# Performance work log

Measured on AMD Instinct MI355X. Metric: run time of the kernel, lower is better.

## Reference

```python
import jax, jax.numpy as jnp
import numpy as np

N_NODES = 100000
N_EDGES = 1600000
EPS = 1e-5


def _xavier(key, shape):
    fan_out, fan_in = shape
    lim = float(np.sqrt(6.0 / (fan_in + fan_out)))
    return jax.random.uniform(key, shape, jnp.float32, -lim, lim)


def setup_inputs() -> dict:
    key = jax.random.key(0)
    ks = jax.random.split(key, 16)
    d_in, d1, d2, d3 = 32, 64, 128, 64
    inp = {
        "x": jax.random.normal(ks[0], (N_NODES, d_in), jnp.float32),
        "edge_index": jax.random.randint(ks[1], (2, N_EDGES), 0, N_NODES, jnp.int64),
        "edge_weight": jax.random.uniform(ks[2], (N_EDGES,), jnp.float32),
        # GraphConv params: lin_rel (with bias) applied to aggregated msgs, lin_root (no bias)
        "W1_rel": _xavier(ks[3], (d1, d_in)), "b1": jnp.zeros((d1,), jnp.float32), "W1_root": _xavier(ks[4], (d1, d_in)),
        "W2_rel": _xavier(ks[5], (d2, d1)), "b2": jnp.zeros((d2,), jnp.float32), "W2_root": _xavier(ks[6], (d2, d1)),
        "W3_rel": _xavier(ks[7], (d3, d2)), "b3": jnp.zeros((d3,), jnp.float32), "W3_root": _xavier(ks[8], (d3, d2)),
        # BatchNorm affine params
        "g1": jnp.ones((d1,), jnp.float32), "be1": jnp.zeros((d1,), jnp.float32),
        "g2": jnp.ones((d2,), jnp.float32), "be2": jnp.zeros((d2,), jnp.float32),
        "g3": jnp.ones((d3,), jnp.float32), "be3": jnp.zeros((d3,), jnp.float32),
        # node-level classifier: Linear(64,32) -> ReLU -> Linear(32,2)
        "Wc1": _xavier(ks[9], (32, d3)), "bc1": jnp.zeros((32,), jnp.float32),
        "Wc2": _xavier(ks[10], (2, 32)), "bc2": jnp.zeros((2,), jnp.float32),
    }
    return inp


def _graph_conv(x, src, dst, W_rel, b, W_root, ew=None):
    msg = x[src]                      # [E, d] gather
    if ew is not None:
        msg = msg * ew[:, None]
    agg = jax.ops.segment_sum(msg, dst, num_segments=N_NODES)  # [N, d] scatter-add
    return agg @ W_rel.T + b + x @ W_root.T


def _bn(h, g, beta):
    mu = jnp.mean(h, axis=0)
    var = jnp.var(h, axis=0)
    return (h - mu) * jax.lax.rsqrt(var + EPS) * g + beta


def reference(x, edge_index, edge_weight,
              W1_rel, b1, W1_root, W2_rel, b2, W2_root, W3_rel, b3, W3_root,
              g1, be1, g2, be2, g3, be3, Wc1, bc1, Wc2, bc2):
    src, dst = edge_index[0], edge_index[1]
    h1 = jax.nn.relu(_bn(_graph_conv(x, src, dst, W1_rel, b1, W1_root), g1, be1))
    h2 = jax.nn.relu(_bn(_graph_conv(h1, src, dst, W2_rel, b2, W2_root), g2, be2))
    h3 = _bn(_graph_conv(h2, src, dst, W3_rel, b3, W3_root, edge_weight), g3, be3)
    h3 = jax.nn.relu(h3 + h1)  # residual (dims match, no projection)
    logits = jax.nn.relu(h3 @ Wc1.T + bc1) @ Wc2.T + bc2  # [N, 2]
    return logits
```

## Files before the change

### kernel.cpp

```cpp
#include <hip/hip_runtime.h>

#define N_NODES 100000
#define N_EDGES 1600000
#define EPSV 1e-5f

__device__ __forceinline__ ushort f2bf(float f) {
  unsigned u = __float_as_uint(f);
  unsigned r = (u + 0x7FFFu + ((u >> 16) & 1u)) >> 16;
  return (ushort)r;
}


#define FILL_SUB 256
#define GRP_W 12500

__global__ void hist_kernel(const int* __restrict__ ei, int* __restrict__ cnt) {
  const int g = blockIdx.x & 7;
  const int sub = blockIdx.x >> 3;
  const int lo = g * GRP_W, hi = lo + GRP_W;
  const int EPB = (N_EDGES + FILL_SUB - 1) / FILL_SUB;
  const int beg = sub * EPB;
  const int end = min(beg + EPB, N_EDGES);
  for (int e = beg + (int)threadIdx.x; e < end; e += (int)blockDim.x) {
    int d = __builtin_nontemporal_load(ei + N_EDGES + e);
    if (d >= lo && d < hi) atomicAdd(&cnt[d], 1);
  }
}

#define SCAN_BLK 1024
#define SCAN_NB ((N_NODES + SCAN_BLK - 1) / SCAN_BLK)

__global__ void scan_phase1(const int* __restrict__ cnt, int* __restrict__ blocksum) {
  __shared__ int part[256];
  int base = blockIdx.x * SCAN_BLK + threadIdx.x * 4;
  int s = 0;
#pragma unroll
  for (int i = 0; i < 4; ++i) {
    int idx = base + i;
    if (idx < N_NODES) s += cnt[idx];
  }
  part[threadIdx.x] = s;
  __syncthreads();
  for (int d = 128; d > 0; d >>= 1) {
    if (threadIdx.x < d) part[threadIdx.x] += part[threadIdx.x + d];
    __syncthreads();
  }
  if (threadIdx.x == 0) blocksum[blockIdx.x] = part[0];
}

__global__ void scan_phase2(int* __restrict__ blocksum, int* __restrict__ rowptr) {
  __shared__ int part[128];
  int tid = threadIdx.x;
  int v = (tid < SCAN_NB) ? blocksum[tid] : 0;
  part[tid] = v;
  __syncthreads();
  for (int d = 1; d < 128; d <<= 1) {
    int t = (tid >= d) ? part[tid - d] : 0;
    __syncthreads();
    part[tid] += t;
    __syncthreads();
  }
  if (tid < SCAN_NB) blocksum[tid] = part[tid] - v;
  if (tid == 127) rowptr[N_NODES] = part[127];
}

__global__ void scan_phase3(const int* __restrict__ cnt, const int* __restrict__ blocksum,
                            int* __restrict__ rowptr, int* __restrict__ cursor) {
  __shared__ int part[256];
  int base = blockIdx.x * SCAN_BLK + threadIdx.x * 4;
  int c[4];
  int s = 0;
#pragma unroll
  for (int i = 0; i < 4; ++i) {
    int idx = base + i;
    c[i] = (idx < N_NODES) ? cnt[idx] : 0;
    s += c[i];
  }
  part[threadIdx.x] = s;
  __syncthreads();
  int me = s;
  for (int d = 1; d < 256; d <<= 1) {
    int t = (threadIdx.x >= d) ? part[threadIdx.x - d] : 0;
    __syncthreads();
    part[threadIdx.x] += t;
    __syncthreads();
  }
  int off = blocksum[blockIdx.x] + part[threadIdx.x] - me;
#pragma unroll
  for (int i = 0; i < 4; ++i) {
    int idx = base + i;
    if (idx < N_NODES) {
      rowptr[idx] = off;
      cursor[idx] = off;
      off += c[i];
    }
  }
}

__global__ void fill_kernel(const int* __restrict__ ei, const float* __restrict__ ew,
                            int* __restrict__ cursor, unsigned* __restrict__ col) {
  const int g = blockIdx.x & 7;
  const int sub = blockIdx.x >> 3;
  const int lo = g * GRP_W, hi = lo + GRP_W;
  const int EPB = (N_EDGES + FILL_SUB - 1) / FILL_SUB;
  const int beg = sub * EPB;
  const int end = min(beg + EPB, N_EDGES);
  for (int e = beg + (int)threadIdx.x; e < end; e += (int)blockDim.x) {
    int d = __builtin_nontemporal_load(ei + N_EDGES + e);
    if (d < lo || d >= hi) continue;
    int p = atomicAdd(&cursor[d], 1);
    int src = __builtin_nontemporal_load(ei + e);
    float w = __builtin_nontemporal_load(ew + e);
    col[p] = ((unsigned)f2bf(w) << 17) | (unsigned)src;
  }
}


__global__ void cast_bf16(const float* __restrict__ in, ushort* __restrict__ out, int n4) {
  int i = blockIdx.x * blockDim.x + threadIdx.x;
  if (i >= n4) return;
  float4 v = reinterpret_cast<const float4*>(in)[i];
  ushort4 o = make_ushort4(f2bf(v.x), f2bf(v.y), f2bf(v.z), f2bf(v.w));
  reinterpret_cast<ushort4*>(out)[i] = o;
}


__global__ void wtrans_kernel(const float* __restrict__ W1rel, const float* __restrict__ W1root,
                              const float* __restrict__ W2rel, const float* __restrict__ W2root,
                              const float* __restrict__ W3rel, const float* __restrict__ W3root,
                              float* __restrict__ Wt) {
  int i = blockIdx.x * blockDim.x + threadIdx.x;
  if (i >= 36864) return;
  float v;
  if (i < 4096) {
    int k = i >> 6, j = i & 63;
    v = (k < 32) ? W1rel[j * 32 + k] : W1root[j * 32 + (k - 32)];
  } else if (i < 20480) {
    int r = i - 4096;
    int k = r >> 7, j = r & 127;
    v = (k < 64) ? W2rel[j * 64 + k] : W2root[j * 64 + (k - 64)];
  } else if (i < 28672) {
    int r = i - 20480;
    int k = r >> 6, j = r & 63;
    v = W3rel[j * 128 + k];
  } else {
    int r = i - 28672;
    int k = r >> 6, j = r & 63;
    v = W3root[j * 128 + k];
  }
  Wt[i] = v;
}


#define SRC_OF(v) ((v) & 0x1FFFFu)
#define W_OF(v) __uint_as_float(((v) >> 17) << 16)

__device__ __forceinline__ unsigned pack2bf(float a, float b) {
  return (unsigned)f2bf(a) | ((unsigned)f2bf(b) << 16);
}

__global__ void gather_d32_bf(const ushort* __restrict__ xb, const int* __restrict__ rowptr,
                              const unsigned* __restrict__ col, ushort* __restrict__ agg) {
  int gid = blockIdx.x * blockDim.x + threadIdx.x;
  int n = gid >> 2;
  if (n >= N_NODES) return;
  int c = gid & 3;
  int beg = rowptr[n], end = rowptr[n + 1];
  float acc[8];
#pragma unroll
  for (int i = 0; i < 8; ++i) acc[i] = 0.f;

  auto body = [&](const uint4& u) {
    unsigned uu[4] = {u.x, u.y, u.z, u.w};
#pragma unroll
    for (int i = 0; i < 4; ++i) {
      acc[2 * i]     += __uint_as_float(uu[i] << 16);
      acc[2 * i + 1] += __uint_as_float(uu[i] & 0xFFFF0000u);
    }
  };

  int p = beg;
  for (; p + 3 < end; p += 4) {
    unsigned e0 = col[p], e1 = col[p + 1], e2 = col[p + 2], e3 = col[p + 3];
    uint4 u0 = *reinterpret_cast<const uint4*>(xb + (size_t)SRC_OF(e0) * 32 + c * 8);
    uint4 u1 = *reinterpret_cast<const uint4*>(xb + (size_t)SRC_OF(e1) * 32 + c * 8);
    uint4 u2 = *reinterpret_cast<const uint4*>(xb + (size_t)SRC_OF(e2) * 32 + c * 8);
    uint4 u3 = *reinterpret_cast<const uint4*>(xb + (size_t)SRC_OF(e3) * 32 + c * 8);
    body(u0); body(u1); body(u2); body(u3);
  }
  for (; p < end; ++p) {
    unsigned e0 = col[p];
    uint4 u0 = *reinterpret_cast<const uint4*>(xb + (size_t)SRC_OF(e0) * 32 + c * 8);
    body(u0);
  }
  uint4 o = make_uint4(pack2bf(acc[0], acc[1]), pack2bf(acc[2], acc[3]),
                       pack2bf(acc[4], acc[5]), pack2bf(acc[6], acc[7]));
  *reinterpret_cast<uint4*>(agg + (size_t)n * 32 + c * 8) = o;
}

template <bool WEIGHTED, bool TRANS, bool OUTB16>
__global__ void gather_d64_bf(const ushort* __restrict__ hb, const int* __restrict__ rowptr,
                              const unsigned* __restrict__ col,
                              const float* __restrict__ sc, const float* __restrict__ sh,
                              void* __restrict__ aggv) {
  int gid = blockIdx.x * blockDim.x + threadIdx.x;
  int n = gid >> 3;
  if (n >= N_NODES) return;
  int c = gid & 7;
  int beg = rowptr[n], end = rowptr[n + 1];
  float sc8[8], sh8[8];
  if (TRANS) {
#pragma unroll
    for (int i = 0; i < 8; ++i) {
      sc8[i] = sc[c * 8 + i];
      sh8[i] = sh[c * 8 + i];
    }
  }
  float acc[8];
#pragma unroll
  for (int i = 0; i < 8; ++i) acc[i] = 0.f;

  auto body = [&](unsigned ev, const uint4& u) {
    float w = WEIGHTED ? W_OF(ev) : 1.f;
    unsigned uu[4] = {u.x, u.y, u.z, u.w};
#pragma unroll
    for (int i = 0; i < 4; ++i) {
      float lo = __uint_as_float(uu[i] << 16);
      float hi = __uint_as_float(uu[i] & 0xFFFF0000u);
      if (TRANS) {
        lo = fmaxf(fmaf(lo, sc8[2 * i], sh8[2 * i]), 0.f);
        hi = fmaxf(fmaf(hi, sc8[2 * i + 1], sh8[2 * i + 1]), 0.f);
      }
      if (WEIGHTED) {
        acc[2 * i]     = fmaf(lo, w, acc[2 * i]);
        acc[2 * i + 1] = fmaf(hi, w, acc[2 * i + 1]);
      } else {
        acc[2 * i]     += lo;
        acc[2 * i + 1] += hi;
      }
    }
  };

  int p = beg;
  for (; p + 3 < end; p += 4) {
    unsigned e0 = col[p], e1 = col[p + 1], e2 = col[p + 2], e3 = col[p + 3];
    uint4 u0 = *reinterpret_cast<const uint4*>(hb + (size_t)SRC_OF(e0) * 64 + c * 8);
    uint4 u1 = *reinterpret_cast<const uint4*>(hb + (size_t)SRC_OF(e1) * 64 + c * 8);
    uint4 u2 = *reinterpret_cast<const uint4*>(hb + (size_t)SRC_OF(e2) * 64 + c * 8);
    uint4 u3 = *reinterpret_cast<const uint4*>(hb + (size_t)SRC_OF(e3) * 64 + c * 8);
    body(e0, u0); body(e1, u1); body(e2, u2); body(e3, u3);
  }
  for (; p < end; ++p) {
    unsigned e0 = col[p];
    uint4 u0 = *reinterpret_cast<const uint4*>(hb + (size_t)SRC_OF(e0) * 64 + c * 8);
    body(e0, u0);
  }
  if constexpr (OUTB16) {
    uint4 o = make_uint4(pack2bf(acc[0], acc[1]), pack2bf(acc[2], acc[3]),
                         pack2bf(acc[4], acc[5]), pack2bf(acc[6], acc[7]));
    *reinterpret_cast<uint4*>((ushort*)aggv + (size_t)n * 64 + c * 8) = o;
  } else {
    float* op = (float*)aggv + (size_t)n * 64 + c * 8;
    *reinterpret_cast<float4*>(op)     = make_float4(acc[0], acc[1], acc[2], acc[3]);
    *reinterpret_cast<float4*>(op + 4) = make_float4(acc[4], acc[5], acc[6], acc[7]);
  }
}


template <int K1, int K2, int DO, int A1B16, int A2B16, int TA1, int TA2, int RADD,
          int STATS, int OUTM>
__global__ __launch_bounds__(256, 4) void gemm_node(
    const void* __restrict__ A1v, const void* __restrict__ A2v,
    const float* __restrict__ Wt,
    const float* __restrict__ sc, const float* __restrict__ sh,
    const float* __restrict__ R, float* __restrict__ out, ushort* __restrict__ outb,
    float* __restrict__ sums) {
  constexpr int K = K1 + K2;
  constexpr int NC = K / 32;
  constexpr int NJB = DO / 64;
  __shared__ __align__(16) float A_lds[64][36];
  __shared__ __align__(16) float W_lds[32][DO];

  const int tid = threadIdx.x;
  const int tx = tid & 15, ty = tid >> 4;
  const int nbase = blockIdx.x * 64;

  float4 acc[4][NJB];
#pragma unroll
  for (int i = 0; i < 4; ++i)
#pragma unroll
    for (int jb = 0; jb < NJB; ++jb) acc[i][jb] = make_float4(0.f, 0.f, 0.f, 0.f);

#pragma unroll 1
  for (int c = 0; c < NC; ++c) {
    const int kb = c * 32;
    if (c) __syncthreads();
#pragma unroll
    for (int it = 0; it < 2; ++it) {
      int idx = it * 256 + tid;
      int nl = idx >> 3;
      int kq = (idx & 7) * 4;
      int k = kb + kq;
      int ng = nbase + nl;
      float4 v = make_float4(0.f, 0.f, 0.f, 0.f);
      bool isA1 = (K2 == 0) || (k < K1);
      if (ng < N_NODES) {
        if (isA1) {
          if constexpr (A1B16) {
            uint2 u = *reinterpret_cast<const uint2*>(
                (const ushort*)A1v + (size_t)ng * K1 + k);
            v.x = __uint_as_float(u.x << 16);
            v.y = __uint_as_float(u.x & 0xFFFF0000u);
            v.z = __uint_as_float(u.y << 16);
            v.w = __uint_as_float(u.y & 0xFFFF0000u);
          } else {
            v = *reinterpret_cast<const float4*>((const float*)A1v + (size_t)ng * K1 + k);
          }
        } else {
          if constexpr (A2B16) {
            uint2 u = *reinterpret_cast<const uint2*>(
                (const ushort*)A2v + (size_t)ng * K2 + (k - K1));
            v.x = __uint_as_float(u.x << 16);
            v.y = __uint_as_float(u.x & 0xFFFF0000u);
            v.z = __uint_as_float(u.y << 16);
            v.w = __uint_as_float(u.y & 0xFFFF0000u);
          } else {
            v = *reinterpret_cast<const float4*>(
                (const float*)A2v + (size_t)ng * K2 + (k - K1));
          }
        }
      }
      if constexpr (TA1) {
        if (isA1) {
          float4 s4 = *reinterpret_cast<const float4*>(sc + k);
          float4 h4 = *reinterpret_cast<const float4*>(sh + k);
          v.x = fmaxf(fmaf(v.x, s4.x, h4.x), 0.f);
          v.y = fmaxf(fmaf(v.y, s4.y, h4.y), 0.f);
          v.z = fmaxf(fmaf(v.z, s4.z, h4.z), 0.f);
          v.w = fmaxf(fmaf(v.w, s4.w, h4.w), 0.f);
        }
      }
      if constexpr (TA2 && K2 > 0) {
        if (!isA1) {
          float4 s4 = *reinterpret_cast<const float4*>(sc + (k - K1));
          float4 h4 = *reinterpret_cast<const float4*>(sh + (k - K1));
          v.x = fmaxf(fmaf(v.x, s4.x, h4.x), 0.f);
          v.y = fmaxf(fmaf(v.y, s4.y, h4.y), 0.f);
          v.z = fmaxf(fmaf(v.z, s4.z, h4.z), 0.f);
          v.w = fmaxf(fmaf(v.w, s4.w, h4.w), 0.f);
        }
      }
      *reinterpret_cast<float4*>(&A_lds[nl][kq]) = v;
    }
    {
      const float4* wsrc = reinterpret_cast<const float4*>(Wt + (size_t)kb * DO);
      float4* wdst = reinterpret_cast<float4*>(&W_lds[0][0]);
#pragma unroll
      for (int it = 0; it < DO / 32; ++it)
        wdst[it * 256 + tid] = wsrc[it * 256 + tid];
    }
    __syncthreads();
#pragma unroll 2
    for (int k4 = 0; k4 < 8; ++k4) {
      float4 a[4];
#pragma unroll
      for (int i = 0; i < 4; ++i)
        a[i] = *reinterpret_cast<const float4*>(&A_lds[ty * 4 + i][k4 * 4]);
#pragma unroll
      for (int q = 0; q < 4; ++q) {
#pragma unroll
        for (int jb = 0; jb < NJB; ++jb) {
          float4 w = *reinterpret_cast<const float4*>(&W_lds[k4 * 4 + q][jb * 64 + tx * 4]);
#pragma unroll
          for (int i = 0; i < 4; ++i) {
            float av = reinterpret_cast<const float*>(&a[i])[q];
            acc[i][jb].x = fmaf(av, w.x, acc[i][jb].x);
            acc[i][jb].y = fmaf(av, w.y, acc[i][jb].y);
            acc[i][jb].z = fmaf(av, w.z, acc[i][jb].z);
            acc[i][jb].w = fmaf(av, w.w, acc[i][jb].w);
          }
        }
      }
    }
  }
#pragma unroll
  for (int i = 0; i < 4; ++i) {
    int ng = nbase + ty * 4 + i;
    if (ng >= N_NODES) continue;
#pragma unroll
    for (int jb = 0; jb < NJB; ++jb) {
      if constexpr (RADD) {
        float4 rr = *reinterpret_cast<const float4*>(R + (size_t)ng * DO + jb * 64 + tx * 4);
        acc[i][jb].x += rr.x; acc[i][jb].y += rr.y;
        acc[i][jb].z += rr.z; acc[i][jb].w += rr.w;
      }
      size_t off = (size_t)ng * DO + jb * 64 + tx * 4;
      if constexpr (OUTM == 1) {
        ushort4 o = make_ushort4(f2bf(acc[i][jb].x), f2bf(acc[i][jb].y),
                                 f2bf(acc[i][jb].z), f2bf(acc[i][jb].w));
        *reinterpret_cast<ushort4*>((ushort*)out + off) = o;
      } else {
        *reinterpret_cast<float4*>(out + off) = acc[i][jb];
        if constexpr (OUTM == 2) {
          ushort4 o = make_ushort4(f2bf(acc[i][jb].x), f2bf(acc[i][jb].y),
                                   f2bf(acc[i][jb].z), f2bf(acc[i][jb].w));
          *reinterpret_cast<ushort4*>(outb + off) = o;
        }
      }
    }
  }
  if constexpr (STATS) {
    __syncthreads();
    float* sums_l = &A_lds[0][0];
    float* sq_l = &W_lds[0][0];
#pragma unroll
    for (int jb = 0; jb < NJB; ++jb) {
      float4 s = make_float4(0.f, 0.f, 0.f, 0.f);
      float4 q = make_float4(0.f, 0.f, 0.f, 0.f);
#pragma unroll
      for (int i = 0; i < 4; ++i) {
        if (nbase + ty * 4 + i < N_NODES) {
          float4 v = acc[i][jb];
          s.x += v.x; s.y += v.y; s.z += v.z; s.w += v.w;
          q.x = fmaf(v.x, v.x, q.x); q.y = fmaf(v.y, v.y, q.y);
          q.z = fmaf(v.z, v.z, q.z); q.w = fmaf(v.w, v.w, q.w);
        }
      }
      *reinterpret_cast<float4*>(&sums_l[ty * DO + jb * 64 + tx * 4]) = s;
      *reinterpret_cast<float4*>(&sq_l[ty * DO + jb * 64 + tx * 4]) = q;
    }
    __syncthreads();
    if (tid < DO) {
      float s = 0.f, q = 0.f;
#pragma unroll
      for (int t = 0; t < 16; ++t) {
        s += sums_l[t * DO + tid];
        q += sq_l[t * DO + tid];
      }
      unsafeAtomicAdd(&sums[tid], s);
      unsafeAtomicAdd(&sums[DO + tid], q);
    }
  }
}


__global__ void bn_finalize(const float* __restrict__ sums, const float* __restrict__ g,
                            const float* __restrict__ be, float* __restrict__ sc,
                            float* __restrict__ sh, int D) {
  int j = threadIdx.x;
  if (j >= D) return;
  const float invN = 1.f / (float)N_NODES;
  float mean = sums[j] * invN;
  float var = sums[D + j] * invN - mean * mean;
  float r = rsqrtf(var + EPSV);
  float scale = g[j] * r;
  sc[j] = scale;
  sh[j] = be[j] - mean * scale;
}


__global__ __launch_bounds__(256) void final_fused(
    const float* __restrict__ h3p, const ushort* __restrict__ h1p,
    const float* __restrict__ sc1, const float* __restrict__ sh1,
    const float* __restrict__ sc3, const float* __restrict__ sh3,
    const float* __restrict__ Wc1, const float* __restrict__ bc1,
    const float* __restrict__ Wc2, const float* __restrict__ bc2,
    float* __restrict__ out) {
  __shared__ __align__(16) float t_lds[64][68];
  __shared__ __align__(16) float w1_lds[64][36];
  __shared__ __align__(16) float c_lds[64][36];
  __shared__ __align__(16) float w2_lds[64];
  __shared__ __align__(16) float b1_lds[32];
  __shared__ float b2_lds[2];
  const int tid = threadIdx.x;
  const int nbase = blockIdx.x * 64;

#pragma unroll
  for (int it = 0; it < 4; ++it) {
    int idx = it * 256 + tid;
    int nl = idx >> 4;
    int k = (idx & 15) * 4;
    int ng = nbase + nl;
    float4 v = make_float4(0.f, 0.f, 0.f, 0.f);
    if (ng < N_NODES) {
      float4 p = *reinterpret_cast<const float4*>(h3p + (size_t)ng * 64 + k);
      uint2 uu = *reinterpret_cast<const uint2*>(h1p + (size_t)ng * 64 + k);
      float ux = __uint_as_float(uu.x << 16);
      float uy = __uint_as_float(uu.x & 0xFFFF0000u);
      float uz = __uint_as_float(uu.y << 16);
      float uw = __uint_as_float(uu.y & 0xFFFF0000u);
      float4 sa = *reinterpret_cast<const float4*>(sc1 + k);
      float4 ha = *reinterpret_cast<const float4*>(sh1 + k);
      float4 sb = *reinterpret_cast<const float4*>(sc3 + k);
      float4 hb = *reinterpret_cast<const float4*>(sh3 + k);
      float h1x = fmaxf(fmaf(ux, sa.x, ha.x), 0.f);
      float h1y = fmaxf(fmaf(uy, sa.y, ha.y), 0.f);
      float h1z = fmaxf(fmaf(uz, sa.z, ha.z), 0.f);
      float h1w = fmaxf(fmaf(uw, sa.w, ha.w), 0.f);
      v.x = fmaxf(fmaf(p.x, sb.x, hb.x) + h1x, 0.f);
      v.y = fmaxf(fmaf(p.y, sb.y, hb.y) + h1y, 0.f);
      v.z = fmaxf(fmaf(p.z, sb.z, hb.z) + h1z, 0.f);
      v.w = fmaxf(fmaf(p.w, sb.w, hb.w) + h1w, 0.f);
    }
    *reinterpret_cast<float4*>(&t_lds[nl][k]) = v;
  }
#pragma unroll
  for (int it = 0; it < 8; ++it) {
    int idx = it * 256 + tid;
    int j = idx >> 6;
    int k = idx & 63;
    w1_lds[k][j] = Wc1[(size_t)j * 64 + k];
  }
  if (tid < 64) w2_lds[tid] = Wc2[tid];
  else if (tid < 96) b1_lds[tid - 64] = bc1[tid - 64];
  else if (tid < 98) b2_lds[tid - 96] = bc2[tid - 96];
  __syncthreads();

  {
    const int tx = tid & 7, ty = tid >> 3;
    float4 a0c = make_float4(0.f, 0.f, 0.f, 0.f);
    float4 a1c = make_float4(0.f, 0.f, 0.f, 0.f);
#pragma unroll 4
    for (int k4 = 0; k4 < 16; ++k4) {
      float4 a0 = *reinterpret_cast<const float4*>(&t_lds[ty * 2 + 0][k4 * 4]);
      float4 a1 = *reinterpret_cast<const float4*>(&t_lds[ty * 2 + 1][k4 * 4]);
#pragma unroll
      for (int q = 0; q < 4; ++q) {
        float4 w = *reinterpret_cast<const float4*>(&w1_lds[k4 * 4 + q][tx * 4]);
        float a0q = reinterpret_cast<const float*>(&a0)[q];
        float a1q = reinterpret_cast<const float*>(&a1)[q];
        a0c.x = fmaf(a0q, w.x, a0c.x); a0c.y = fmaf(a0q, w.y, a0c.y);
        a0c.z = fmaf(a0q, w.z, a0c.z); a0c.w = fmaf(a0q, w.w, a0c.w);
        a1c.x = fmaf(a1q, w.x, a1c.x); a1c.y = fmaf(a1q, w.y, a1c.y);
        a1c.z = fmaf(a1q, w.z, a1c.z); a1c.w = fmaf(a1q, w.w, a1c.w);
      }
    }
    float4 b = *reinterpret_cast<const float4*>(&b1_lds[tx * 4]);
    a0c.x = fmaxf(a0c.x + b.x, 0.f); a0c.y = fmaxf(a0c.y + b.y, 0.f);
    a0c.z = fmaxf(a0c.z + b.z, 0.f); a0c.w = fmaxf(a0c.w + b.w, 0.f);
    a1c.x = fmaxf(a1c.x + b.x, 0.f); a1c.y = fmaxf(a1c.y + b.y, 0.f);
    a1c.z = fmaxf(a1c.z + b.z, 0.f); a1c.w = fmaxf(a1c.w + b.w, 0.f);
    *reinterpret_cast<float4*>(&c_lds[ty * 2 + 0][tx * 4]) = a0c;
    *reinterpret_cast<float4*>(&c_lds[ty * 2 + 1][tx * 4]) = a1c;
  }
  __syncthreads();

  if (tid < 128) {
    int nl = tid >> 1, o = tid & 1;
    int ng = nbase + nl;
    if (ng < N_NODES) {
      float s = b2_lds[o];
#pragma unroll
      for (int k = 0; k < 32; ++k) s = fmaf(c_lds[nl][k], w2_lds[o * 32 + k], s);
      out[(size_t)ng * 2 + o] = s;
    }
  }
}


extern "C" void kernel_launch(void* const* d_in, const int* in_sizes, int n_in,
                              void* d_out, int out_size, void* d_ws, size_t ws_size,
                              hipStream_t stream) {
  const float* x      = (const float*)d_in[0];
  const int*   ei     = (const int*)d_in[1];
  const float* ew     = (const float*)d_in[2];
  const float* W1rel  = (const float*)d_in[3];
  const float* W1root = (const float*)d_in[5];
  const float* W2rel  = (const float*)d_in[6];
  const float* W2root = (const float*)d_in[8];
  const float* W3rel  = (const float*)d_in[9];
  const float* W3root = (const float*)d_in[11];
  const float* g1  = (const float*)d_in[12];
  const float* be1 = (const float*)d_in[13];
  const float* g2  = (const float*)d_in[14];
  const float* be2 = (const float*)d_in[15];
  const float* g3  = (const float*)d_in[16];
  const float* be3 = (const float*)d_in[17];
  const float* Wc1 = (const float*)d_in[18];
  const float* bc1 = (const float*)d_in[19];
  const float* Wc2 = (const float*)d_in[20];
  const float* bc2 = (const float*)d_in[21];

  float* ws = (float*)d_ws;
  const size_t NF = (size_t)N_NODES * 64;
  float* A = ws;
  float* B = ws + NF;
  float* C = ws + 2 * NF;
  float* E = ws + 3 * NF;
  float* X = ws + 5 * NF;
  float* S = X;
  int* rowptr   = (int*)(X + 1024);
  int* cnt      = rowptr + (N_NODES + 2);
  int* cursor   = cnt + N_NODES;
  int* blocksum = cursor + N_NODES;
  unsigned* col = (unsigned*)(blocksum + 128);
  float* Wt     = (float*)(col + N_EDGES);
  float* Wt1  = Wt;
  float* Wt2  = Wt + 4096;
  float* Wt3r = Wt + 20480;
  float* Wt3o = Wt + 28672;

  ushort* agg1b  = (ushort*)A;
  ushort* agg2b  = (ushort*)A;
  ushort* xb     = (ushort*)B;
  ushort* y2b    = (ushort*)B;
  ushort* h1preb = (ushort*)C;
  ushort* h2preb = (ushort*)E;

  hipMemsetAsync(S, 0, 1024 * sizeof(float), stream);
  hipMemsetAsync(cnt, 0, N_NODES * sizeof(int), stream);

  const int tileBlocks = (N_NODES + 63) / 64;

  cast_bf16<<<(N_NODES * 32 / 4 + 255) / 256, 256, 0, stream>>>(x, xb, N_NODES * 32 / 4);
  wtrans_kernel<<<144, 256, 0, stream>>>(W1rel, W1root, W2rel, W2root, W3rel, W3root, Wt);

  hist_kernel<<<8 * FILL_SUB, 256, 0, stream>>>(ei, cnt);
  scan_phase1<<<SCAN_NB, 256, 0, stream>>>(cnt, blocksum);
  scan_phase2<<<1, 128, 0, stream>>>(blocksum, rowptr);
  scan_phase3<<<SCAN_NB, 256, 0, stream>>>(cnt, blocksum, rowptr, cursor);
  fill_kernel<<<8 * FILL_SUB, 256, 0, stream>>>(ei, ew, cursor, col);

  gather_d32_bf<<<(N_NODES * 4 + 255) / 256, 256, 0, stream>>>(xb, rowptr, col, agg1b);
  gemm_node<32, 32, 64, 1, 1, 0, 0, 0, 1, 1><<<tileBlocks, 256, 0, stream>>>(
      agg1b, xb, Wt1, nullptr, nullptr, nullptr, (float*)h1preb, nullptr, S);
  bn_finalize<<<1, 128, 0, stream>>>(S, g1, be1, S + 128, S + 192, 64);

  gather_d64_bf<false, true, true><<<(N_NODES * 8 + 255) / 256, 256, 0, stream>>>(
      h1preb, rowptr, col, S + 128, S + 192, agg2b);
  gemm_node<64, 64, 128, 1, 1, 0, 1, 0, 1, 1><<<tileBlocks, 256, 0, stream>>>(
      agg2b, h1preb, Wt2, S + 128, S + 192, nullptr, (float*)h2preb, nullptr, S + 256);
  bn_finalize<<<1, 128, 0, stream>>>(S + 256, g2, be2, S + 512, S + 640, 128);

  gemm_node<128, 0, 64, 1, 0, 1, 0, 0, 0, 1><<<tileBlocks, 256, 0, stream>>>(
      h2preb, nullptr, Wt3r, S + 512, S + 640, nullptr, (float*)y2b, nullptr, nullptr);

  gather_d64_bf<true, false, false><<<(N_NODES * 8 + 255) / 256, 256, 0, stream>>>(
      y2b, rowptr, col, nullptr, nullptr, A);
  gemm_node<128, 0, 64, 1, 0, 1, 0, 1, 1, 0><<<tileBlocks, 256, 0, stream>>>(
      h2preb, nullptr, Wt3o, S + 512, S + 640, A, B, nullptr, S + 768);
  bn_finalize<<<1, 128, 0, stream>>>(S + 768, g3, be3, S + 896, S + 960, 64);

  final_fused<<<tileBlocks, 256, 0, stream>>>(B, h1preb, S + 128, S + 192, S + 896, S + 960,
                                              Wc1, bc1, Wc2, bc2, (float*)d_out);
}
```

Baseline: 471.6 us.

## Fuse layer-3 rel/root GEMMs and fold root term into weighted gather

Layer 3's rel and root projections now run as one 128-wide GEMM over h2 that writes two bf16 outputs: y2 for the gather and z3 for the root term. The weighted gather adds z3 in its epilogue and stores h3pre as bf16. A new small kernel computes the BN3 statistics from that buffer, and final_fused reads bf16 instead of fp32. This removes one full pass over h2 and the fp32 intermediate traffic, at the cost of an extra stats pass and bf16 rounding of h3pre. The hist and fill kernels also switch to strided uint4 vector loads of the destination indices.

```diff
diff --git a/kernel.cpp b/kernel.cpp
--- a/kernel.cpp
+++ b/kernel.cpp
@@ -18,12 +18,14 @@
   const int g = blockIdx.x & 7;
   const int sub = blockIdx.x >> 3;
   const int lo = g * GRP_W, hi = lo + GRP_W;
-  const int EPB = (N_EDGES + FILL_SUB - 1) / FILL_SUB;
-  const int beg = sub * EPB;
-  const int end = min(beg + EPB, N_EDGES);
-  for (int e = beg + (int)threadIdx.x; e < end; e += (int)blockDim.x) {
-    int d = __builtin_nontemporal_load(ei + N_EDGES + e);
-    if (d >= lo && d < hi) atomicAdd(&cnt[d], 1);
+  const uint4* dst4 = reinterpret_cast<const uint4*>(ei + N_EDGES);
+  const int NV = N_EDGES / 4;
+  for (int i = sub * 256 + (int)threadIdx.x; i < NV; i += FILL_SUB * 256) {
+    uint4 d4 = dst4[i];
+    int dd[4] = {(int)d4.x, (int)d4.y, (int)d4.z, (int)d4.w};
+#pragma unroll
+    for (int j = 0; j < 4; ++j)
+      if (dd[j] >= lo && dd[j] < hi) atomicAdd(&cnt[dd[j]], 1);
   }
 }
 
@@ -102,16 +104,21 @@
   const int g = blockIdx.x & 7;
   const int sub = blockIdx.x >> 3;
   const int lo = g * GRP_W, hi = lo + GRP_W;
-  const int EPB = (N_EDGES + FILL_SUB - 1) / FILL_SUB;
-  const int beg = sub * EPB;
-  const int end = min(beg + EPB, N_EDGES);
-  for (int e = beg + (int)threadIdx.x; e < end; e += (int)blockDim.x) {
-    int d = __builtin_nontemporal_load(ei + N_EDGES + e);
-    if (d < lo || d >= hi) continue;
-    int p = atomicAdd(&cursor[d], 1);
-    int src = __builtin_nontemporal_load(ei + e);
-    float w = __builtin_nontemporal_load(ew + e);
-    col[p] = ((unsigned)f2bf(w) << 17) | (unsigned)src;
+  const uint4* dst4 = reinterpret_cast<const uint4*>(ei + N_EDGES);
+  const int NV = N_EDGES / 4;
+  for (int i = sub * 256 + (int)threadIdx.x; i < NV; i += FILL_SUB * 256) {
+    uint4 d4 = dst4[i];
+    int dd[4] = {(int)d4.x, (int)d4.y, (int)d4.z, (int)d4.w};
+#pragma unroll
+    for (int j = 0; j < 4; ++j) {
+      if (dd[j] >= lo && dd[j] < hi) {
+        int e = i * 4 + j;
+        int p = atomicAdd(&cursor[dd[j]], 1);
+        int src = __builtin_nontemporal_load(ei + e);
+        float w = __builtin_nontemporal_load(ew + e);
+        col[p] = ((unsigned)f2bf(w) << 17) | (unsigned)src;
+      }
+    }
   }
 }
 
@@ -139,14 +146,10 @@
     int r = i - 4096;
     int k = r >> 7, j = r & 127;
     v = (k < 64) ? W2rel[j * 64 + k] : W2root[j * 64 + (k - 64)];
-  } else if (i < 28672) {
+  } else {
     int r = i - 20480;
-    int k = r >> 6, j = r & 63;
-    v = W3rel[j * 128 + k];
-  } else {
-    int r = i - 28672;
-    int k = r >> 6, j = r & 63;
-    v = W3root[j * 128 + k];
+    int k = r >> 7, j = r & 127;
+    v = (j < 64) ? W3rel[(size_t)j * 128 + k] : W3root[(size_t)(j - 64) * 128 + k];
   }
   Wt[i] = v;
 }
@@ -198,11 +201,11 @@
   *reinterpret_cast<uint4*>(agg + (size_t)n * 32 + c * 8) = o;
 }
 
-template <bool WEIGHTED, bool TRANS, bool OUTB16>
+template <bool WEIGHTED, bool TRANS, bool OUTB16, bool ADDZ>
 __global__ void gather_d64_bf(const ushort* __restrict__ hb, const int* __restrict__ rowptr,
                               const unsigned* __restrict__ col,
                               const float* __restrict__ sc, const float* __restrict__ sh,
-                              void* __restrict__ aggv) {
+                              const ushort* __restrict__ zb, void* __restrict__ aggv) {
   int gid = blockIdx.x * blockDim.x + threadIdx.x;
   int n = gid >> 3;
   if (n >= N_NODES) return;
@@ -254,6 +257,15 @@
     unsigned e0 = col[p];
     uint4 u0 = *reinterpret_cast<const uint4*>(hb + (size_t)SRC_OF(e0) * 64 + c * 8);
     body(e0, u0);
+  }
+  if constexpr (ADDZ) {
+    uint4 z = *reinterpret_cast<const uint4*>(zb + (size_t)n * 64 + c * 8);
+    unsigned zz[4] = {z.x, z.y, z.z, z.w};
+#pragma unroll
+    for (int i = 0; i < 4; ++i) {
+      acc[2 * i]     += __uint_as_float(zz[i] << 16);
+      acc[2 * i + 1] += __uint_as_float(zz[i] & 0xFFFF0000u);
+    }
   }
   if constexpr (OUTB16) {
     uint4 o = make_uint4(pack2bf(acc[0], acc[1]), pack2bf(acc[2], acc[3]),
@@ -394,17 +406,24 @@
         acc[i][jb].x += rr.x; acc[i][jb].y += rr.y;
         acc[i][jb].z += rr.z; acc[i][jb].w += rr.w;
       }
-      size_t off = (size_t)ng * DO + jb * 64 + tx * 4;
-      if constexpr (OUTM == 1) {
+      if constexpr (OUTM == 4) {
         ushort4 o = make_ushort4(f2bf(acc[i][jb].x), f2bf(acc[i][jb].y),
                                  f2bf(acc[i][jb].z), f2bf(acc[i][jb].w));
-        *reinterpret_cast<ushort4*>((ushort*)out + off) = o;
+        ushort* dst = (jb == 0) ? (ushort*)out : outb;
+        *reinterpret_cast<ushort4*>(dst + (size_t)ng * 64 + tx * 4) = o;
       } else {
-        *reinterpret_cast<float4*>(out + off) = acc[i][jb];
-        if constexpr (OUTM == 2) {
+        size_t off = (size_t)ng * DO + jb * 64 + tx * 4;
+        if constexpr (OUTM == 1) {
           ushort4 o = make_ushort4(f2bf(acc[i][jb].x), f2bf(acc[i][jb].y),
                                    f2bf(acc[i][jb].z), f2bf(acc[i][jb].w));
-          *reinterpret_cast<ushort4*>(outb + off) = o;
+          *reinterpret_cast<ushort4*>((ushort*)out + off) = o;
+        } else {
+          *reinterpret_cast<float4*>(out + off) = acc[i][jb];
+          if constexpr (OUTM == 2) {
+            ushort4 o = make_ushort4(f2bf(acc[i][jb].x), f2bf(acc[i][jb].y),
+                                     f2bf(acc[i][jb].z), f2bf(acc[i][jb].w));
+            *reinterpret_cast<ushort4*>(outb + off) = o;
+          }
         }
       }
     }
@@ -440,6 +459,31 @@
       unsafeAtomicAdd(&sums[tid], s);
       unsafeAtomicAdd(&sums[DO + tid], q);
     }
+  }
+}
+
+
+__global__ void bn_stats_bf(const ushort* __restrict__ h, float* __restrict__ sums) {
+  __shared__ float sl[256], ql[256];
+  int j = threadIdx.x & 63;
+  int lane = threadIdx.x >> 6;
+  float s = 0.f, q = 0.f;
+  for (int n = blockIdx.x * 4 + lane; n < N_NODES; n += gridDim.x * 4) {
+    float v = __uint_as_float((unsigned)h[(size_t)n * 64 + j] << 16);
+    s += v;
+    q = fmaf(v, v, q);
+  }
+  sl[threadIdx.x] = s;
+  ql[threadIdx.x] = q;
+  __syncthreads();
+  if (threadIdx.x < 64) {
+#pragma unroll
+    for (int t = 1; t < 4; ++t) {
+      s += sl[t * 64 + j];
+      q += ql[t * 64 + j];
+    }
+    unsafeAtomicAdd(&sums[j], s);
+    unsafeAtomicAdd(&sums[64 + j], q);
   }
 }
 
@@ -460,7 +504,7 @@
 
 
 __global__ __launch_bounds__(256) void final_fused(
-    const float* __restrict__ h3p, const ushort* __restrict__ h1p,
+    const ushort* __restrict__ h3p, const ushort* __restrict__ h1p,
     const float* __restrict__ sc1, const float* __restrict__ sh1,
     const float* __restrict__ sc3, const float* __restrict__ sh3,
     const float* __restrict__ Wc1, const float* __restrict__ bc1,
@@ -483,7 +527,11 @@
     int ng = nbase + nl;
     float4 v = make_float4(0.f, 0.f, 0.f, 0.f);
     if (ng < N_NODES) {
-      float4 p = *reinterpret_cast<const float4*>(h3p + (size_t)ng * 64 + k);
+      uint2 pp = *reinterpret_cast<const uint2*>(h3p + (size_t)ng * 64 + k);
+      float px = __uint_as_float(pp.x << 16);
+      float py = __uint_as_float(pp.x & 0xFFFF0000u);
+      float pz = __uint_as_float(pp.y << 16);
+      float pw = __uint_as_float(pp.y & 0xFFFF0000u);
       uint2 uu = *reinterpret_cast<const uint2*>(h1p + (size_t)ng * 64 + k);
       float ux = __uint_as_float(uu.x << 16);
       float uy = __uint_as_float(uu.x & 0xFFFF0000u);
@@ -497,10 +545,10 @@
       float h1y = fmaxf(fmaf(uy, sa.y, ha.y), 0.f);
       float h1z = fmaxf(fmaf(uz, sa.z, ha.z), 0.f);
       float h1w = fmaxf(fmaf(uw, sa.w, ha.w), 0.f);
-      v.x = fmaxf(fmaf(p.x, sb.x, hb.x) + h1x, 0.f);
-      v.y = fmaxf(fmaf(p.y, sb.y, hb.y) + h1y, 0.f);
-      v.z = fmaxf(fmaf(p.z, sb.z, hb.z) + h1z, 0.f);
-      v.w = fmaxf(fmaf(p.w, sb.w, hb.w) + h1w, 0.f);
+      v.x = fmaxf(fmaf(px, sb.x, hb.x) + h1x, 0.f);
+      v.y = fmaxf(fmaf(py, sb.y, hb.y) + h1y, 0.f);
+      v.z = fmaxf(fmaf(pz, sb.z, hb.z) + h1z, 0.f);
+      v.w = fmaxf(fmaf(pw, sb.w, hb.w) + h1w, 0.f);
     }
     *reinterpret_cast<float4*>(&t_lds[nl][k]) = v;
   }
@@ -597,13 +645,14 @@
   float* Wt     = (float*)(col + N_EDGES);
   float* Wt1  = Wt;
   float* Wt2  = Wt + 4096;
-  float* Wt3r = Wt + 20480;
-  float* Wt3o = Wt + 28672;
+  float* Wt3c = Wt + 20480;
 
   ushort* agg1b  = (ushort*)A;
   ushort* agg2b  = (ushort*)A;
+  ushort* h3preb = (ushort*)A;
   ushort* xb     = (ushort*)B;
   ushort* y2b    = (ushort*)B;
+  ushort* z3b    = (ushort*)B + NF;
   ushort* h1preb = (ushort*)C;
   ushort* h2preb = (ushort*)E;
 
@@ -626,21 +675,21 @@
       agg1b, xb, Wt1, nullptr, nullptr, nullptr, (float*)h1preb, nullptr, S);
   bn_finalize<<<1, 128, 0, stream>>>(S, g1, be1, S + 128, S + 192, 64);
 
-  gather_d64_bf<false, true, true><<<(N_NODES * 8 + 255) / 256, 256, 0, stream>>>(
-      h1preb, rowptr, col, S + 128, S + 192, agg2b);
+  gather_d64_bf<false, true, true, false><<<(N_NODES * 8 + 255) / 256, 256, 0, stream>>>(
+      h1preb, rowptr, col, S + 128, S + 192, nullptr, agg2b);
   gemm_node<64, 64, 128, 1, 1, 0, 1, 0, 1, 1><<<tileBlocks, 256, 0, stream>>>(
       agg2b, h1preb, Wt2, S + 128, S + 192, nullptr, (float*)h2preb, nullptr, S + 256);
   bn_finalize<<<1, 128, 0, stream>>>(S + 256, g2, be2, S + 512, S + 640, 128);
 
-  gemm_node<128, 0, 64, 1, 0, 1, 0, 0, 0, 1><<<tileBlocks, 256, 0, stream>>>(
-      h2preb, nullptr, Wt3r, S + 512, S + 640, nullptr, (float*)y2b, nullptr, nullptr);
-
-  gather_d64_bf<true, false, false><<<(N_NODES * 8 + 255) / 256, 256, 0, stream>>>(
-      y2b, rowptr, col, nullptr, nullptr, A);
-  gemm_node<128, 0, 64, 1, 0, 1, 0, 1, 1, 0><<<tileBlocks, 256, 0, stream>>>(
-      h2preb, nullptr, Wt3o, S + 512, S + 640, A, B, nullptr, S + 768);
+  gemm_node<128, 0, 128, 1, 0, 1, 0, 0, 0, 4><<<tileBlocks, 256, 0, stream>>>(
+      h2preb, nullptr, Wt3c, S + 512, S + 640, nullptr, (float*)y2b, z3b, nullptr);
+
+  gather_d64_bf<true, false, true, true><<<(N_NODES * 8 + 255) / 256, 256, 0, stream>>>(
+      y2b, rowptr, col, nullptr, nullptr, z3b, h3preb);
+  bn_stats_bf<<<128, 256, 0, stream>>>(h3preb, S + 768);
   bn_finalize<<<1, 128, 0, stream>>>(S + 768, g3, be3, S + 896, S + 960, 64);
 
-  final_fused<<<tileBlocks, 256, 0, stream>>>(B, h1preb, S + 128, S + 192, S + 896, S + 960,
-                                              Wc1, bc1, Wc2, bc2, (float*)d_out);
-}
+  final_fused<<<tileBlocks, 256, 0, stream>>>(h3preb, h1preb, S + 128, S + 192,
+                                              S + 896, S + 960, Wc1, bc1, Wc2, bc2,
+                                              (float*)d_out);
+}
```

Result: slower. 495.4 us (+5.0%).
